# Kernel optimization log

Hardware: AMD Instinct MI355X
Metric: run time of the kernel (lower is better)

The kernel has to match this reference:

```python
import jax, jax.numpy as jnp
import numpy as np

BS, N_STK, N_STK_PNT = 4, 32, 128
N_PNT = N_STK * N_STK_PNT
SP_IN, DN_IN = 128, 128
SP_OUT, DN_OUT = 256, 256
SP_NEAR, DN_NEAR = 2, 10
COOR = 128


def _conv2d(x, w, b, stride=(1, 1), pad='VALID'):
    # x [bs,C,H,W], w [O,I,kh,kw]
    y = jax.lax.conv_general_dilated(x, w, window_strides=stride, padding=pad,
                                     dimension_numbers=('NCHW', 'OIHW', 'NCHW'))
    return y + b[None, :, None, None]


def _fps(xyz, n_sample):
    # farthest point sampling. xyz [bs,n,c] -> [bs,n_sample] int32
    n = xyz.shape[1]

    def one(x):
        def body(i, state):
            idx, dist, far = state
            idx = idx.at[i].set(far)
            d = jnp.sum((x - x[far]) ** 2, axis=-1)
            dist = jnp.minimum(dist, d)
            return idx, dist, jnp.argmax(dist).astype(jnp.int32)

        idx0 = jnp.zeros((n_sample,), jnp.int32)
        dist0 = jnp.full((n,), 1e10, x.dtype)
        idx, _, _ = jax.lax.fori_loop(0, n_sample, body, (idx0, dist0, jnp.int32(0)))
        return idx

    return jax.vmap(one)(xyz)


def _gcn(x, W, b, g, bt, k):
    # DGCNN edge-conv. x [bs,c,n]; W [2c,co]
    xt = jnp.swapaxes(x, 1, 2)                                   # [bs,n,c]
    sq = jnp.sum(xt * xt, axis=-1)                               # [bs,n]
    dist = sq[:, :, None] - 2.0 * jnp.einsum('bnc,bmc->bnm', xt, xt) + sq[:, None, :]
    _, idx = jax.lax.top_k(-dist, k)                             # [bs,n,k]
    nbr = jax.vmap(lambda p, i: p[i])(xt, idx)                   # [bs,n,k,c]
    ctr = jnp.broadcast_to(xt[:, :, None, :], nbr.shape)
    edge = jnp.concatenate([ctr, nbr - ctr], axis=-1)            # [bs,n,k,2c]
    h = jnp.einsum('bnke,eo->bnko', edge, W) + b
    h = jax.nn.relu(g * h + bt)
    return jnp.swapaxes(jnp.max(h, axis=2), 1, 2)                # [bs,co,n]


def setup_inputs() -> dict:
    key = jax.random.key(0)
    ks = jax.random.split(key, 16)
    f32 = jnp.float32
    d = {
        'sparse_fea': jax.random.normal(ks[0], (BS, SP_IN, N_STK), f32),
        'dense_fea': jax.random.normal(ks[1], (BS, DN_IN, N_PNT), f32),
        'stk_coor': jax.random.normal(ks[2], (BS, N_STK, COOR), f32),
        # DenseToSparse: Conv2d(dn_in->dn_in, (1,3)) + BN
        'd2s_w': jax.random.normal(ks[3], (DN_IN, DN_IN, 1, 3), f32) * 0.05,
        'd2s_b': jnp.zeros((DN_IN,), f32),
        'd2s_g': jnp.ones((DN_IN,), f32),
        'd2s_bt': jnp.zeros((DN_IN,), f32),
        # sparse GCN: in = SP_IN + DN_IN, edge feat 2*in
        'sp_W': jax.random.normal(ks[4], (2 * (SP_IN + DN_IN), SP_OUT), f32) * 0.05,
        'sp_b': jnp.zeros((SP_OUT,), f32),
        'sp_g': jnp.ones((SP_OUT,), f32),
        'sp_bt': jnp.zeros((SP_OUT,), f32),
        # dense GCN: in = DN_IN + SP_IN
        'dn_W': jax.random.normal(ks[5], (2 * (DN_IN + SP_IN), DN_OUT), f32) * 0.05,
        'dn_b': jnp.zeros((DN_OUT,), f32),
        'dn_g': jnp.ones((DN_OUT,), f32),
        'dn_bt': jnp.zeros((DN_OUT,), f32),
        # DownSample: Conv2d(dn_out->dn_out, (1,3), stride (1,2), pad (0,1)) + BN
        'ds_w': jax.random.normal(ks[6], (DN_OUT, DN_OUT, 1, 3), f32) * 0.05,
        'ds_b': jnp.zeros((DN_OUT,), f32),
        'ds_g': jnp.ones((DN_OUT,), f32),
        'ds_bt': jnp.zeros((DN_OUT,), f32),
    }
    return d


def reference(sparse_fea, dense_fea, stk_coor,
              d2s_w, d2s_b, d2s_g, d2s_bt,
              sp_W, sp_b, sp_g, sp_bt,
              dn_W, dn_b, dn_g, dn_bt,
              ds_w, ds_b, ds_g, ds_bt):
    bs = sparse_fea.shape[0]
    df = dense_fea.reshape(bs, DN_IN, N_STK, N_STK_PNT)
    # DenseToSparse: conv (1,3) valid + BN(eval) + relu + max over stroke points
    h = _conv2d(df, d2s_w, d2s_b)
    h = jax.nn.relu(d2s_g[None, :, None, None] * h + d2s_bt[None, :, None, None])
    sp_from_dn = jnp.max(h, axis=3)                                    # [bs,dn_in,n_stk]
    union_sparse = jnp.concatenate([sparse_fea, sp_from_dn], axis=1)   # [bs,sp_in+dn_in,n_stk]
    # SparseToDense: broadcast stroke feature onto its points
    dn_from_sp = jnp.broadcast_to(sparse_fea[:, :, :, None], (bs, SP_IN, N_STK, N_STK_PNT))
    union_dense = jnp.concatenate([df, dn_from_sp], axis=1).reshape(bs, DN_IN + SP_IN, N_PNT)
    # GCN (DGCNN edge conv) updates
    sparse_up = _gcn(union_sparse, sp_W, sp_b, sp_g, sp_bt, SP_NEAR)   # [bs,SP_OUT,n_stk]
    dense_up = _gcn(union_dense, dn_W, dn_b, dn_g, dn_bt, DN_NEAR)     # [bs,DN_OUT,n_pnt]
    # DownSample: FPS on stroke coords, gather strokes, strided conv on points
    n_half = N_STK // 2
    fps_idx = _fps(stk_coor, n_half)                                   # [bs,n_half]
    stk_coor_s = jnp.take_along_axis(stk_coor, fps_idx[:, :, None], axis=1)
    sp_s = jnp.take_along_axis(jnp.swapaxes(sparse_up, 1, 2), fps_idx[:, :, None], axis=1)
    sp_s = jnp.swapaxes(sp_s, 1, 2)                                    # [bs,SP_OUT,n_half]
    dn = dense_up.reshape(bs, DN_OUT, N_STK, N_STK_PNT)
    dn = jnp.take_along_axis(dn, fps_idx[:, None, :, None], axis=2)    # [bs,DN_OUT,n_half,n_stk_pnt]
    dn = _conv2d(dn, ds_w, ds_b, stride=(1, 2), pad=[(0, 0), (1, 1)])
    dn = jax.nn.relu(ds_g[None, :, None, None] * dn + ds_bt[None, :, None, None])
    dn = dn.reshape(bs, DN_OUT, n_half * (N_STK_PNT // 2))
    return sp_s, dn, stk_coor_s
```

## Files before the change

### kernel.cpp

```cpp
#include <hip/hip_runtime.h>

#define NPNT 4096
#define NSTK 32

typedef _Float16 half8 __attribute__((ext_vector_type(8)));
typedef float f32x4 __attribute__((ext_vector_type(4)));
typedef unsigned long long u64;

static const size_t OFF_XT   = 0;
static const size_t OFF_P    = 4194304;
static const size_t OFF_Q    = 8388608;
static const size_t OFF_SQD  = 12582912;
static const size_t OFF_SPFD = 12599296;
static const size_t OFF_XS   = 12615680;
static const size_t OFF_PS   = 12648448;
static const size_t OFF_QS   = 12681216;
static const size_t OFF_WSP  = 12746752;
static const size_t OFF_KNN  = 13402112;
static const size_t OFF_IDXS = 13565952;
static const size_t OFF_FPS  = 13566208;
static const size_t OFF_SD   = 13566272;

__device__ __forceinline__ bool lexlt(float d1, int i1, float d2, int i2) {
  return (d1 < d2) || (d1 == d2 && i1 < i2);
}
__device__ __forceinline__ void insert10(float ld[10], int li[10], float d, int i) {
  if (!lexlt(d, i, ld[9], li[9])) return;
  ld[9] = d; li[9] = i;
#pragma unroll
  for (int j = 9; j > 0; j--) {
    if (lexlt(ld[j], li[j], ld[j-1], li[j-1])) {
      float td = ld[j]; ld[j] = ld[j-1]; ld[j-1] = td;
      int ti = li[j]; li[j] = li[j-1]; li[j-1] = ti;
    }
  }
}

__device__ __forceinline__ void insertK(u64 lk[10], u64 k) {
  if (k >= lk[9]) return;
  lk[9] = k;
#pragma unroll
  for (int j = 9; j > 0; j--) {
    u64 a = lk[j-1], b2 = lk[j];
    bool sw = b2 < a;
    lk[j-1] = sw ? b2 : a;
    lk[j]   = sw ? a : b2;
  }
}

#define CASK(a, b) { u64 _x = (a), _y = (b); bool _s = _y < _x; \
  (a) = _s ? _y : _x; (b) = _s ? _x : _y; }

__device__ __forceinline__ void merge10(u64 lk[10], const u64 b[10]) {
  u64 c[10];
#pragma unroll
  for (int i = 0; i < 10; i++) { u64 t = b[9 - i]; u64 a = lk[i]; c[i] = a < t ? a : t; }
  CASK(c[0], c[5]); CASK(c[1], c[6]); CASK(c[2], c[7]); CASK(c[3], c[8]); CASK(c[4], c[9]);
  CASK(c[0], c[1]); CASK(c[1], c[2]); CASK(c[2], c[3]); CASK(c[3], c[4]);
  CASK(c[0], c[1]); CASK(c[1], c[2]); CASK(c[2], c[3]);
  CASK(c[0], c[1]); CASK(c[1], c[2]);
  CASK(c[0], c[1]);
  CASK(c[5], c[6]); CASK(c[6], c[7]); CASK(c[7], c[8]); CASK(c[8], c[9]);
  CASK(c[5], c[6]); CASK(c[6], c[7]); CASK(c[7], c[8]);
  CASK(c[5], c[6]); CASK(c[6], c[7]);
  CASK(c[5], c[6]);
#pragma unroll
  for (int i = 0; i < 10; i++) lk[i] = c[i];
}

__global__ __launch_bounds__(256) void k_split256(const float* __restrict__ df, const float* __restrict__ sf,
    _Float16* __restrict__ XH, _Float16* __restrict__ XL, float* __restrict__ sqd) {
  int b = blockIdx.x, n0 = blockIdx.y * 64;
  int t = threadIdx.x;
  int s0 = n0 >> 7;
  __shared__ float T[128][68];
  __shared__ _Float16 Sh[128], Sl[128];
  {
    int c = t >> 1, nh = (t & 1) * 32;
    const float* src = &df[((size_t)b * 128 + c) * NPNT + n0 + nh];
#pragma unroll
    for (int j = 0; j < 8; j++) *(float4*)&T[c][nh + j * 4] = *(const float4*)&src[j * 4];
  }
  if (t < 128) {
    float x = sf[((size_t)b * 128 + t) * NSTK + s0];
    _Float16 hi = (_Float16)x;
    Sh[t] = hi; Sl[t] = (_Float16)(x - (float)hi);
  }
  __syncthreads();
  {
    int n = t >> 2, cseg = (t & 3) * 32;
    size_t base = ((size_t)b * NPNT + n0 + n) * 256;
    float s = 0.0f;
#pragma unroll
    for (int k = 0; k < 4; k++) {
      half8 hv, lv, shv, slv;
#pragma unroll
      for (int e = 0; e < 8; e++) {
        float x = T[cseg + k * 8 + e][n];
        s = fmaf(x, x, s);
        _Float16 hi = (_Float16)x;
        hv[e] = hi; lv[e] = (_Float16)(x - (float)hi);
        shv[e] = Sh[cseg + k * 8 + e];
        slv[e] = Sl[cseg + k * 8 + e];
      }
      *(half8*)&XH[base + cseg + k * 8] = hv;
      *(half8*)&XL[base + cseg + k * 8] = lv;
      *(half8*)&XH[base + 128 + cseg + k * 8] = shv;
      *(half8*)&XL[base + 128 + cseg + k * 8] = slv;
    }
    s += __shfl_xor(s, 1);
    s += __shfl_xor(s, 2);
    if ((t & 3) == 0) sqd[(size_t)b * NPNT + n0 + n] = s;
  }
}

__global__ __launch_bounds__(256) void k_splitW(const float* __restrict__ W,
    _Float16* __restrict__ WPh, _Float16* __restrict__ WPl,
    _Float16* __restrict__ WQh, _Float16* __restrict__ WQl) {
  int k = blockIdx.x, o = threadIdx.x;
  float w1 = W[(size_t)k * 256 + o];
  float w2 = W[(size_t)(k + 256) * 256 + o];
  float p = w1 - w2;
  _Float16 ph = (_Float16)p;  WPh[(size_t)o * 256 + k] = ph;
  WPl[(size_t)o * 256 + k] = (_Float16)(p - (float)ph);
  _Float16 qh = (_Float16)w2; WQh[(size_t)o * 256 + k] = qh;
  WQl[(size_t)o * 256 + k] = (_Float16)(w2 - (float)qh);
}

__global__ __launch_bounds__(256) void k_d2s(const float* __restrict__ df, const float* __restrict__ w,
    const float* __restrict__ cb, const float* __restrict__ g, const float* __restrict__ bt,
    float* __restrict__ spfd) {
  int b = blockIdx.x, o0 = blockIdx.y * 64, s = blockIdx.z;
  int n0 = s * 128;
  int t = threadIdx.x;
  __shared__ float A[96][64];
  __shared__ float Bs[32][132];
  float acc[4][8];
#pragma unroll
  for (int i = 0; i < 4; i++)
#pragma unroll
    for (int j = 0; j < 8; j++) acc[i][j] = 0.0f;
  int tn = t & 15, to = t >> 4;
  for (int ic = 0; ic < 128; ic += 32) {
    {
      int ol = t >> 2, q = t & 3;
      const float* src = &w[((size_t)(o0 + ol) * 128 + ic) * 3 + q * 24];
#pragma unroll
      for (int r = 0; r < 6; r++) {
        float4 v = *(const float4*)&src[r * 4];
        int e = q * 24 + r * 4;
        A[e+0][ol] = v.x; A[e+1][ol] = v.y; A[e+2][ol] = v.z; A[e+3][ol] = v.w;
      }
    }
    for (int idx = t; idx < 32 * 33; idx += 256) {
      int row = idx / 33, f4 = idx % 33;
      int nb = n0 + f4 * 4;
      const float* srow = &df[((size_t)b * 128 + ic + row) * NPNT];
      float4 v;
      if (nb + 3 < NPNT) v = *(const float4*)&srow[nb];
      else {
        v.x = srow[nb   < NPNT ? nb   : NPNT-1];
        v.y = srow[nb+1 < NPNT ? nb+1 : NPNT-1];
        v.z = srow[nb+2 < NPNT ? nb+2 : NPNT-1];
        v.w = srow[nb+3 < NPNT ? nb+3 : NPNT-1];
      }
      *(float4*)&Bs[row][f4 * 4] = v;
    }
    __syncthreads();
#pragma unroll 2
    for (int ii = 0; ii < 32; ii++) {
      float bv[12];
      *(float4*)&bv[0] = *(const float4*)&Bs[ii][tn * 8];
      *(float4*)&bv[4] = *(const float4*)&Bs[ii][tn * 8 + 4];
      *(float4*)&bv[8] = *(const float4*)&Bs[ii][tn * 8 + 8];
#pragma unroll
      for (int kw = 0; kw < 3; kw++) {
        float4 av = *(const float4*)&A[ii * 3 + kw][to * 4];
#pragma unroll
        for (int j = 0; j < 8; j++) {
          float bvj = bv[kw + j];
          acc[0][j] = fmaf(av.x, bvj, acc[0][j]);
          acc[1][j] = fmaf(av.y, bvj, acc[1][j]);
          acc[2][j] = fmaf(av.z, bvj, acc[2][j]);
          acc[3][j] = fmaf(av.w, bvj, acc[3][j]);
        }
      }
    }
    __syncthreads();
  }
  __shared__ float Dr[64][17];
#pragma unroll
  for (int i = 0; i < 4; i++) {
    int o = o0 + to * 4 + i;
    float gg = g[o], bb = cb[o], bo = bt[o];
    float m = 0.0f;
#pragma unroll
    for (int j = 0; j < 8; j++) {
      int p = tn * 8 + j;
      if (p < 126) {
        float v = fmaf(gg, acc[i][j] + bb, bo);
        v = v > 0.0f ? v : 0.0f;
        m = v > m ? v : m;
      }
    }
    Dr[to * 4 + i][tn] = m;
  }
  __syncthreads();
  if (t < 64) {
    float m = 0.0f;
#pragma unroll
    for (int k = 0; k < 16; k++) m = Dr[t][k] > m ? Dr[t][k] : m;
    spfd[((size_t)b * 128 + o0 + t) * NSTK + s] = m;
  }
}

__global__ __launch_bounds__(128) void k_fps(const float* __restrict__ coor, int* __restrict__ fpsidx,
                                             float* __restrict__ out2) {
  int b = blockIdx.x, t = threadIdx.x;
  __shared__ float X[32][132];
  __shared__ float dist[32];
  __shared__ int far_s;
  __shared__ int sel[16];
  for (int idx = t; idx < 32 * 32; idx += 128) {
    int r = idx >> 5, q = idx & 31;
    *(float4*)&X[r][q * 4] = *(const float4*)&coor[((size_t)b * 32 + r) * 128 + q * 4];
  }
  if (t < 32) dist[t] = 1e10f;
  if (t == 0) far_s = 0;
  __syncthreads();
  for (int it = 0; it < 16; it++) {
    int far = far_s;
    if (t == 0) sel[it] = far;
    if (t < 32) {
      float d = 0.0f;
      for (int c = 0; c < 128; c++) { float dd = X[t][c] - X[far][c]; d = fmaf(dd, dd, d); }
      float dm = dist[t];
      dist[t] = d < dm ? d : dm;
    }
    __syncthreads();
    if (t == 0) {
      float best = -1.0f; int bi = 0;
      for (int m = 0; m < 32; m++) if (dist[m] > best) { best = dist[m]; bi = m; }
      far_s = bi;
    }
    __syncthreads();
  }
  if (t < 16) fpsidx[b * 16 + t] = sel[t];
  __syncthreads();
  for (int idx = t; idx < 16 * 32; idx += 128) {
    int j = idx >> 5, q = idx & 31;
    *(float4*)&out2[((size_t)b * 16 + j) * 128 + q * 4] = *(const float4*)&X[sel[j]][q * 4];
  }
}

__global__ __launch_bounds__(256) void k_sparse_graph(const float* __restrict__ sf, const float* __restrict__ spfd,
    float* __restrict__ xs, int* __restrict__ idxs, float* __restrict__ SD) {
  int b = blockIdx.x, t = threadIdx.x;
  __shared__ float X[32][260];
  __shared__ float sq[32];
  __shared__ float D[32][33];
  for (int idx = t; idx < 32 * 256; idx += 256) {
    int n = idx >> 8, c = idx & 255;
    float v = (c < 128) ? sf[((size_t)b * 128 + c) * NSTK + n]
                        : spfd[((size_t)b * 128 + (c - 128)) * NSTK + n];
    X[n][c] = v;
  }
  __syncthreads();
  for (int idx = t; idx < 32 * 64; idx += 256) {
    int n = idx >> 6, q = idx & 63;
    *(float4*)&xs[((size_t)b * 32 + n) * 256 + q * 4] = *(const float4*)&X[n][q * 4];
  }
#pragma unroll
  for (int rep = 0; rep < 4; rep++) {
    int p = t + rep * 256;
    int s = p >> 5, u = p & 31;
    float acc = 0.0f;
    for (int c = 0; c < 128; c++) {
      float d = X[s][c] - X[u][c];
      acc = fmaf(d, d, acc);
    }
    SD[(size_t)b * 1024 + p] = acc;
  }
  if (t < 32) {
    float s = 0.0f;
    for (int c = 0; c < 256; c++) s = fmaf(X[t][c], X[t][c], s);
    sq[t] = s;
  }
  __syncthreads();
  {
    int n = t >> 3;
    for (int mg = 0; mg < 4; mg++) {
      int m = (t & 7) + mg * 8;
      float dot = 0.0f;
      for (int c = 0; c < 256; c++) dot = fmaf(X[n][c], X[m][c], dot);
      D[n][m] = (sq[n] - 2.0f * dot) + sq[m];
    }
  }
  __syncthreads();
  if (t < 32) {
    float d0 = 1e30f, d1 = 1e30f; int i0 = 0, i1 = 0;
    for (int m = 0; m < 32; m++) {
      float d = D[t][m];
      if (d < d0) { d1 = d0; i1 = i0; d0 = d; i0 = m; }
      else if (d < d1) { d1 = d; i1 = m; }
    }
    idxs[(b * 32 + t) * 2 + 0] = i0;
    idxs[(b * 32 + t) * 2 + 1] = i1;
  }
}

__global__ __launch_bounds__(256) void k_sparse_pq(const float* __restrict__ xs, const float* __restrict__ W,
    float* __restrict__ Ps, float* __restrict__ Qs) {
  int b = blockIdx.x >> 5, n = blockIdx.x & 31;
  int o = threadIdx.x;
  const float* xr = &xs[((size_t)b * 32 + n) * 256];
  float accP = 0.0f, accQ = 0.0f;
  for (int c = 0; c < 256; c++) {
    float xc = xr[c];
    float w1 = W[(size_t)c * 256 + o];
    float w2 = W[(size_t)(c + 256) * 256 + o];
    accP = fmaf(xc, w1 - w2, accP);
    accQ = fmaf(xc, w2, accQ);
  }
  Ps[((size_t)b * 32 + n) * 256 + o] = accP;
  Qs[((size_t)b * 32 + n) * 256 + o] = accQ;
}

__global__ __launch_bounds__(256) void k_sparse_cg(const float* __restrict__ Ps, const float* __restrict__ Qs,
    const int* __restrict__ idxs, const int* __restrict__ fps,
    const float* __restrict__ g, const float* __restrict__ cb, const float* __restrict__ bt,
    float* __restrict__ out0) {
  int b = blockIdx.x, j = blockIdx.y, o = threadIdx.x;
  int n = fps[b * 16 + j];
  int i0 = idxs[(b * 32 + n) * 2 + 0], i1 = idxs[(b * 32 + n) * 2 + 1];
  float p = Ps[((size_t)b * 32 + n) * 256 + o];
  float q0 = Qs[((size_t)b * 32 + i0) * 256 + o];
  float q1 = Qs[((size_t)b * 32 + i1) * 256 + o];
  float gg = g[o], bb = cb[o], bo = bt[o];
  float h0 = fmaf(gg, p + q0 + bb, bo); h0 = h0 > 0.0f ? h0 : 0.0f;
  float h1 = fmaf(gg, p + q1 + bb, bo); h1 = h1 > 0.0f ? h1 : 0.0f;
  out0[((size_t)b * 256 + o) * 16 + j] = h0 > h1 ? h0 : h1;
}

#define STAGE(ch2_, p_) { \
  int srow = t >> 2, scol = (t & 3) * 16; \
  size_t gp = (bofs + (size_t)(m0 + (ch2_) * 64 + srow)) * 256 + (p_) * 64 + scol; \
  float4 gh0 = *(const float4*)&XH[gp]; float4 gh1 = *(const float4*)&XH[gp + 8]; \
  float4 gl0 = *(const float4*)&XL[gp]; float4 gl1 = *(const float4*)&XL[gp + 8]; \
  int lo = srow * 72 + scol; \
  *(float4*)&BshH[lo] = gh0; *(float4*)&BshH[lo + 8] = gh1; \
  *(float4*)&BshL[lo] = gl0; *(float4*)&BshL[lo + 8] = gl1; }

#define DWU(wv_, r_, c_) DwU[(((wv_) * 16 + (r_)) * 68) + (c_)]

__global__ __launch_bounds__(256, 4) void k_knn_mfma(const _Float16* __restrict__ XH,
    const _Float16* __restrict__ XL, const float* __restrict__ sqd, const float* __restrict__ SD,
    const int* __restrict__ fps, u64* __restrict__ pk) {
  const int h = blockIdx.x, rb = blockIdx.y, b = blockIdx.z;
  const int t = threadIdx.x;
  const int w = t >> 6, L = t & 63;
  const int c15 = L & 15, q = L >> 4;
  const int jst = rb >> 1;
  const int ph = (rb & 1) * 64;
  const int s_stk = fps[b * 16 + jst];
  const int nsrc = s_stk * 128 + ph + w * 16;
  const int rc0 = rb * 64 + w * 16;
  const size_t bofs = (size_t)b * NPNT;

  __shared__ __align__(16) char SMEM[18432];
  _Float16* const BshH = (_Float16*)SMEM;
  _Float16* const BshL = (_Float16*)(SMEM + 64 * 72 * 2);
  unsigned* const DwU = (unsigned*)SMEM;

  half8 ah[4], al[4];
  {
    const _Float16* ap  = XH + (bofs + nsrc + c15) * 256 + q * 8;
    const _Float16* apl = XL + (bofs + nsrc + c15) * 256 + q * 8;
#pragma unroll
    for (int ch = 0; ch < 4; ch++) {
      ah[ch] = *(const half8*)(ap + ch * 32);
      al[ch] = *(const half8*)(apl + ch * 32);
    }
  }
  float snr[4];
#pragma unroll
  for (int r = 0; r < 4; r++) snr[r] = sqd[bofs + nsrc + q * 4 + r];

  u64 lk[10];
#pragma unroll
  for (int j = 0; j < 10; j++) lk[j] = ~0ull;

  const bool own_here = ((s_stk >> 1) == h);
  const int r_sel = L >> 2, sl = L & 3;
  const int u0 = own_here ? s_stk : (h * 2);
  const int u1 = own_here ? (s_stk ^ 1) : (h * 2 + 1);

#pragma unroll 1
  for (int it = 0; it < 2; it++) {
    const int u = (it == 0) ? u0 : u1;
    const int m0 = u * 128;
    const float SDv = SD[((size_t)b * 32 + s_stk) * 32 + u];

#pragma unroll 1
    for (int ch2 = 0; ch2 < 2; ch2++) {
      float smv[4];
#pragma unroll
      for (int cg = 0; cg < 4; cg++) smv[cg] = sqd[bofs + m0 + ch2 * 64 + cg * 16 + c15];

      f32x4 zz = {0.0f, 0.0f, 0.0f, 0.0f};
      f32x4 acc[4];
#pragma unroll
      for (int cg = 0; cg < 4; cg++) acc[cg] = zz;

      __syncthreads();
      STAGE(ch2, 0);
      __syncthreads();
#pragma unroll
      for (int chl = 0; chl < 2; chl++) {
#pragma unroll
        for (int cg = 0; cg < 4; cg++) {
          int lo = (cg * 16 + c15) * 72 + chl * 32 + q * 8;
          half8 bh = *(const half8*)&BshH[lo];
          half8 bl = *(const half8*)&BshL[lo];
          acc[cg] = __builtin_amdgcn_mfma_f32_16x16x32_f16(ah[chl], bh, acc[cg], 0, 0, 0);
          acc[cg] = __builtin_amdgcn_mfma_f32_16x16x32_f16(ah[chl], bl, acc[cg], 0, 0, 0);
          acc[cg] = __builtin_amdgcn_mfma_f32_16x16x32_f16(al[chl], bh, acc[cg], 0, 0, 0);
        }
      }
      __syncthreads();
      STAGE(ch2, 1);
      __syncthreads();
#pragma unroll
      for (int chl = 0; chl < 2; chl++) {
#pragma unroll
        for (int cg = 0; cg < 4; cg++) {
          int lo = (cg * 16 + c15) * 72 + chl * 32 + q * 8;
          half8 bh = *(const half8*)&BshH[lo];
          half8 bl = *(const half8*)&BshL[lo];
          acc[cg] = __builtin_amdgcn_mfma_f32_16x16x32_f16(ah[2 + chl], bh, acc[cg], 0, 0, 0);
          acc[cg] = __builtin_amdgcn_mfma_f32_16x16x32_f16(ah[2 + chl], bl, acc[cg], 0, 0, 0);
          acc[cg] = __builtin_amdgcn_mfma_f32_16x16x32_f16(al[2 + chl], bh, acc[cg], 0, 0, 0);
        }
      }
      __syncthreads();

#pragma unroll
      for (int cg = 0; cg < 4; cg++) {
        float basec = SDv + smv[cg];
#pragma unroll
        for (int r = 0; r < 4; r++) {
          float d = fmaf(-2.0f, acc[cg][r], snr[r] + basec);
          unsigned uu = __float_as_uint(d);
          unsigned kk = uu ^ ((unsigned)((int)uu >> 31) | 0x80000000u);
          DWU(w, q * 4 + r, cg * 16 + c15) = kk;
        }
      }
#pragma unroll
      for (int jj = 0; jj < 4; jj++) {
        uint4 kv = *(const uint4*)&DWU(w, r_sel, jj * 16 + sl * 4);
        int ib = m0 + ch2 * 64 + jj * 16 + sl * 4;
        insertK(lk, ((u64)kv.x << 32) | (unsigned)(ib + 0));
        insertK(lk, ((u64)kv.y << 32) | (unsigned)(ib + 1));
        insertK(lk, ((u64)kv.z << 32) | (unsigned)(ib + 2));
        insertK(lk, ((u64)kv.w << 32) | (unsigned)(ib + 3));
      }
    }
  }

#pragma unroll
  for (int m = 1; m <= 2; m <<= 1) {
    u64 o[10];
#pragma unroll
    for (int j = 0; j < 10; j++) o[j] = __shfl_xor(lk[j], m);
    merge10(lk, o);
  }
  if (sl == 0) {
    size_t row = (size_t)b * 2048 + rc0 + r_sel;
    u64* dst = &pk[(row * 16 + h) * 10];
#pragma unroll
    for (int j = 0; j < 10; j++) dst[j] = lk[j];
  }
}

__global__ __launch_bounds__(256) void k_knn_merge(const u64* __restrict__ pk,
                                                   int* __restrict__ knnc) {
  size_t row = blockIdx.x * 256 + threadIdx.x;
  const u64* src = &pk[row * 160];
  u64 lk[10];
#pragma unroll
  for (int j = 0; j < 10; j++) lk[j] = src[j];
#pragma unroll
  for (int l = 1; l < 16; l++) {
    u64 bv[10];
#pragma unroll
    for (int j = 0; j < 10; j++) bv[j] = src[l * 10 + j];
    merge10(lk, bv);
  }
#pragma unroll
  for (int j = 0; j < 10; j++) knnc[row * 10 + j] = (int)(unsigned)(lk[j] & 0xffffffffull);
}

__global__ __launch_bounds__(256, 2) void k_pq_mfma(const _Float16* __restrict__ XH, const _Float16* __restrict__ XL,
    const _Float16* __restrict__ WPh, const _Float16* __restrict__ WPl,
    const _Float16* __restrict__ WQh, const _Float16* __restrict__ WQl,
    const int* __restrict__ fps, const float* __restrict__ g, const float* __restrict__ cb,
    const float* __restrict__ bt, float* __restrict__ Pc, float* __restrict__ Qp) {
  const int b = blockIdx.z;
  const int t = threadIdx.x, w = t >> 6, L = t & 63;
  const int c15 = L & 15, q = L >> 4;
  const int ow = blockIdx.y * 128 + (w >> 1) * 64;
  const size_t bofs = (size_t)b * NPNT;
  f32x4 zz = {0.0f, 0.0f, 0.0f, 0.0f};

  {
    const int nw = blockIdx.x * 32 + (w & 1) * 16;
    f32x4 accQ[4];
#pragma unroll
    for (int cg = 0; cg < 4; cg++) accQ[cg] = zz;
    const _Float16* ap  = XH + (bofs + nw + c15) * 256 + q * 8;
    const _Float16* apl = XL + (bofs + nw + c15) * 256 + q * 8;
#pragma unroll
    for (int ch = 0; ch < 8; ch++) {
      half8 a_h = *(const half8*)(ap + ch * 32);
      half8 a_l = *(const half8*)(apl + ch * 32);
#pragma unroll
      for (int cg = 0; cg < 4; cg++) {
        size_t wb = (size_t)(ow + cg * 16 + c15) * 256 + ch * 32 + q * 8;
        half8 bqh = *(const half8*)(WQh + wb);
        half8 bql = *(const half8*)(WQl + wb);
        accQ[cg] = __builtin_amdgcn_mfma_f32_16x16x32_f16(a_h, bqh, accQ[cg], 0, 0, 0);
        accQ[cg] = __builtin_amdgcn_mfma_f32_16x16x32_f16(a_h, bql, accQ[cg], 0, 0, 0);
        accQ[cg] = __builtin_amdgcn_mfma_f32_16x16x32_f16(a_l, bqh, accQ[cg], 0, 0, 0);
      }
    }
#pragma unroll
    for (int cg = 0; cg < 4; cg++) {
      int o = ow + cg * 16 + c15;
      float gg = g[o];
#pragma unroll
      for (int r = 0; r < 4; r++) {
        Qp[(bofs + nw + q * 4 + r) * 256 + o] = gg * accQ[cg][r];
      }
    }
  }

  if (blockIdx.x < 64) {
    const int m0 = blockIdx.x * 32 + (w & 1) * 16;
    const int jst = m0 >> 7;
    const int pbase = m0 & 127;
    const int nsrc = fps[b * 16 + jst] * 128 + pbase;
    f32x4 accP[4];
#pragma unroll
    for (int cg = 0; cg < 4; cg++) accP[cg] = zz;
    const _Float16* ap  = XH + (bofs + nsrc + c15) * 256 + q * 8;
    const _Float16* apl = XL + (bofs + nsrc + c15) * 256 + q * 8;
#pragma unroll
    for (int ch = 0; ch < 8; ch++) {
      half8 a_h = *(const half8*)(ap + ch * 32);
      half8 a_l = *(const half8*)(apl + ch * 32);
#pragma unroll
      for (int cg = 0; cg < 4; cg++) {
        size_t wb = (size_t)(ow + cg * 16 + c15) * 256 + ch * 32 + q * 8;
        half8 bph = *(const half8*)(WPh + wb);
        half8 bpl = *(const half8*)(WPl + wb);
        accP[cg] = __builtin_amdgcn_mfma_f32_16x16x32_f16(a_h, bph, accP[cg], 0, 0, 0);
        accP[cg] = __builtin_amdgcn_mfma_f32_16x16x32_f16(a_h, bpl, accP[cg], 0, 0, 0);
        accP[cg] = __builtin_amdgcn_mfma_f32_16x16x32_f16(a_l, bph, accP[cg], 0, 0, 0);
      }
    }
#pragma unroll
    for (int cg = 0; cg < 4; cg++) {
      int o = ow + cg * 16 + c15;
      float gg = g[o], bb = cb[o], bo = bt[o];
#pragma unroll
      for (int r = 0; r < 4; r++) {
        Pc[(((size_t)b * 16 + jst) * 128 + pbase + q * 4 + r) * 256 + o] =
            fmaf(gg, accP[cg][r] + bb, bo);
      }
    }
  }
}

__global__ __launch_bounds__(256) void k_build_E(const float* __restrict__ Pc, const float* __restrict__ Qp,
    const int* __restrict__ knnc, float* __restrict__ E) {
  int pp = blockIdx.x, j = blockIdx.y, b = blockIdx.z;
  int t = threadIdx.x;
  float v[3];
#pragma unroll
  for (int dp = 0; dp < 3; dp++) {
    int p = 2 * pp - 1 + dp;
    float val = 0.0f;
    if (p >= 0 && p < 128) {
      size_t m = ((size_t)b * 16 + j) * 128 + p;
      float pv = Pc[m * 256 + t];
      const int* id = &knnc[m * 10];
      float mx = 0.0f;
#pragma unroll
      for (int k = 0; k < 10; k++) {
        float qv = Qp[((size_t)b * NPNT + id[k]) * 256 + t];
        float h = pv + qv;
        mx = h > mx ? h : mx;
      }
      val = mx;
    }
    v[dp] = val;
  }
  size_t base = ((size_t)(b * 16 + j) * 64 + pp) * 768;
  E[base + 3 * t + 0] = v[0];
  E[base + 3 * t + 1] = v[1];
  E[base + 3 * t + 2] = v[2];
}

__global__ __launch_bounds__(256) void k_ds_gemm(const float* __restrict__ Wd, const float* __restrict__ E,
    const float* __restrict__ cb, const float* __restrict__ g, const float* __restrict__ bt,
    float* __restrict__ out1) {
  int j0 = blockIdx.x * 64, o0 = blockIdx.y * 64, b = blockIdx.z;
  int t = threadIdx.x;
  __shared__ float A[32][68];
  __shared__ float Bs[32][68];
  float acc[4][4];
#pragma unroll
  for (int i = 0; i < 4; i++)
#pragma unroll
    for (int j = 0; j < 4; j++) acc[i][j] = 0.0f;
  int tj = t & 15, to = t >> 4;
  for (int kc = 0; kc < 768; kc += 32) {
    {
      int ol = t >> 2, q = t & 3;
      const float* src = &Wd[(size_t)(o0 + ol) * 768 + kc + q * 8];
      float4 v0 = *(const float4*)src, v1 = *(const float4*)(src + 4);
      int cc = q * 8;
      A[cc+0][ol] = v0.x; A[cc+1][ol] = v0.y; A[cc+2][ol] = v0.z; A[cc+3][ol] = v0.w;
      A[cc+4][ol] = v1.x; A[cc+5][ol] = v1.y; A[cc+6][ol] = v1.z; A[cc+7][ol] = v1.w;
    }
    {
      int jl = t >> 2, q = t & 3;
      const float* src = &E[((size_t)b * 1024 + j0 + jl) * 768 + kc + q * 8];
      float4 v0 = *(const float4*)src, v1 = *(const float4*)(src + 4);
      int cc = q * 8;
      Bs[cc+0][jl] = v0.x; Bs[cc+1][jl] = v0.y; Bs[cc+2][jl] = v0.z; Bs[cc+3][jl] = v0.w;
      Bs[cc+4][jl] = v1.x; Bs[cc+5][jl] = v1.y; Bs[cc+6][jl] = v1.z; Bs[cc+7][jl] = v1.w;
    }
    __syncthreads();
#pragma unroll 4
    for (int k = 0; k < 32; k++) {
      float4 a = *(const float4*)&A[k][to * 4];
      float4 bv = *(const float4*)&Bs[k][tj * 4];
      float av[4] = {a.x, a.y, a.z, a.w};
      float bb[4] = {bv.x, bv.y, bv.z, bv.w};
#pragma unroll
      for (int i = 0; i < 4; i++)
#pragma unroll
        for (int j = 0; j < 4; j++)
          acc[i][j] = fmaf(av[i], bb[j], acc[i][j]);
    }
    __syncthreads();
  }
#pragma unroll
  for (int i = 0; i < 4; i++) {
    int o = o0 + to * 4 + i;
    float gg = g[o], bb = cb[o], bo = bt[o];
    float4 v;
    float x0 = fmaf(gg, acc[i][0] + bb, bo); v.x = x0 > 0.0f ? x0 : 0.0f;
    float x1 = fmaf(gg, acc[i][1] + bb, bo); v.y = x1 > 0.0f ? x1 : 0.0f;
    float x2 = fmaf(gg, acc[i][2] + bb, bo); v.z = x2 > 0.0f ? x2 : 0.0f;
    float x3 = fmaf(gg, acc[i][3] + bb, bo); v.w = x3 > 0.0f ? x3 : 0.0f;
    *(float4*)&out1[((size_t)b * 256 + o) * 1024 + j0 + tj * 4] = v;
  }
}

extern "C" void kernel_launch(void* const* d_in, const int* in_sizes, int n_in,
                              void* d_out, int out_size, void* d_ws, size_t ws_size,
                              hipStream_t stream) {
  (void)in_sizes; (void)n_in; (void)out_size; (void)ws_size;
  const float* sf    = (const float*)d_in[0];
  const float* df    = (const float*)d_in[1];
  const float* coor  = (const float*)d_in[2];
  const float* d2sw  = (const float*)d_in[3];
  const float* d2sb  = (const float*)d_in[4];
  const float* d2sg  = (const float*)d_in[5];
  const float* d2sbt = (const float*)d_in[6];
  const float* spW   = (const float*)d_in[7];
  const float* spb   = (const float*)d_in[8];
  const float* spg   = (const float*)d_in[9];
  const float* spbt  = (const float*)d_in[10];
  const float* dnW   = (const float*)d_in[11];
  const float* dnb   = (const float*)d_in[12];
  const float* dng   = (const float*)d_in[13];
  const float* dnbt  = (const float*)d_in[14];
  const float* dsw   = (const float*)d_in[15];
  const float* dsb   = (const float*)d_in[16];
  const float* dsg   = (const float*)d_in[17];
  const float* dsbt  = (const float*)d_in[18];

  float* ws   = (float*)d_ws;
  float* Pc   = ws + OFF_P;
  float* Qp   = ws + OFF_Q;
  float* SQD  = ws + OFF_SQD;
  float* SPFD = ws + OFF_SPFD;
  float* XS   = ws + OFF_XS;
  float* PS   = ws + OFF_PS;
  float* QS   = ws + OFF_QS;
  int*   KNNC = (int*)(ws + OFF_KNN);
  int*   IDXS = (int*)(ws + OFF_IDXS);
  int*   FPS  = (int*)(ws + OFF_FPS);
  float* SD   = ws + OFF_SD;
  _Float16* XT2H = (_Float16*)(ws + OFF_XT);
  _Float16* XT2L = XT2H + (size_t)4 * NPNT * 256;
  float* E = ws + OFF_XT;
  _Float16* WPh = (_Float16*)(ws + OFF_WSP);
  _Float16* WPl = WPh + 65536;
  _Float16* WQh = WPh + 131072;
  _Float16* WQl = WPh + 196608;
  u64* PK = (u64*)(ws + OFF_Q);

  float* out0 = (float*)d_out;
  float* out1 = out0 + 16384;
  float* out2 = out1 + 1048576;

  k_split256<<<dim3(4, 64), 256, 0, stream>>>(df, sf, XT2H, XT2L, SQD);
  k_splitW<<<dim3(256), 256, 0, stream>>>(dnW, WPh, WPl, WQh, WQl);
  k_d2s<<<dim3(4, 2, 32), 256, 0, stream>>>(df, d2sw, d2sb, d2sg, d2sbt, SPFD);
  k_fps<<<dim3(4), 128, 0, stream>>>(coor, FPS, out2);
  k_sparse_graph<<<dim3(4), 256, 0, stream>>>(sf, SPFD, XS, IDXS, SD);
  k_sparse_pq<<<dim3(128), 256, 0, stream>>>(XS, spW, PS, QS);
  k_sparse_cg<<<dim3(4, 16), 256, 0, stream>>>(PS, QS, IDXS, FPS, spg, spb, spbt, out0);
  k_knn_mfma<<<dim3(16, 32, 4), 256, 0, stream>>>(XT2H, XT2L, SQD, SD, FPS, PK);
  k_knn_merge<<<dim3(32), 256, 0, stream>>>(PK, KNNC);
  k_pq_mfma<<<dim3(128, 2, 4), 256, 0, stream>>>(XT2H, XT2L, WPh, WPl, WQh, WQl,
                                                 FPS, dng, dnb, dnbt, Pc, Qp);
  k_build_E<<<dim3(64, 16, 4), 256, 0, stream>>>(Pc, Qp, KNNC, E);
  k_ds_gemm<<<dim3(16, 4, 4), 256, 0, stream>>>(dsw, E, dsb, dsg, dsbt, out1);
}
```

Measured before the change: 455.7 us.

## Fuse four preprocessing kernels into one launch and parallelize kNN merge across lanes

Merges the split, weight-split, dense-to-sparse conv and FPS kernels into a single k_pre kernel that dispatches on block index, so the four independent jobs share one launch and run concurrently. It also spreads the 16-way partial top-10 merge in k_knn_merge over four lanes per row with shuffle-based merges, giving 4x more threads. The fused kernel's shared memory is sized for the largest branch, which may reduce occupancy for the lighter branches, and the serial FPS blocks now sit in the same grid as the others.

```diff
diff --git a/kernel.cpp b/kernel.cpp
--- a/kernel.cpp
+++ b/kernel.cpp
@@ -21,21 +21,6 @@
 static const size_t OFF_FPS  = 13566208;
 static const size_t OFF_SD   = 13566272;
 
-__device__ __forceinline__ bool lexlt(float d1, int i1, float d2, int i2) {
-  return (d1 < d2) || (d1 == d2 && i1 < i2);
-}
-__device__ __forceinline__ void insert10(float ld[10], int li[10], float d, int i) {
-  if (!lexlt(d, i, ld[9], li[9])) return;
-  ld[9] = d; li[9] = i;
-#pragma unroll
-  for (int j = 9; j > 0; j--) {
-    if (lexlt(ld[j], li[j], ld[j-1], li[j-1])) {
-      float td = ld[j]; ld[j] = ld[j-1]; ld[j-1] = td;
-      int ti = li[j]; li[j] = li[j-1]; li[j-1] = ti;
-    }
-  }
-}
-
 __device__ __forceinline__ void insertK(u64 lk[10], u64 k) {
   if (k >= lk[9]) return;
   lk[9] = k;
@@ -68,188 +53,191 @@
   for (int i = 0; i < 10; i++) lk[i] = c[i];
 }
 
-__global__ __launch_bounds__(256) void k_split256(const float* __restrict__ df, const float* __restrict__ sf,
-    _Float16* __restrict__ XH, _Float16* __restrict__ XL, float* __restrict__ sqd) {
-  int b = blockIdx.x, n0 = blockIdx.y * 64;
-  int t = threadIdx.x;
-  int s0 = n0 >> 7;
-  __shared__ float T[128][68];
-  __shared__ _Float16 Sh[128], Sl[128];
-  {
-    int c = t >> 1, nh = (t & 1) * 32;
-    const float* src = &df[((size_t)b * 128 + c) * NPNT + n0 + nh];
-#pragma unroll
-    for (int j = 0; j < 8; j++) *(float4*)&T[c][nh + j * 4] = *(const float4*)&src[j * 4];
-  }
-  if (t < 128) {
-    float x = sf[((size_t)b * 128 + t) * NSTK + s0];
-    _Float16 hi = (_Float16)x;
-    Sh[t] = hi; Sl[t] = (_Float16)(x - (float)hi);
-  }
-  __syncthreads();
-  {
-    int n = t >> 2, cseg = (t & 3) * 32;
-    size_t base = ((size_t)b * NPNT + n0 + n) * 256;
-    float s = 0.0f;
-#pragma unroll
-    for (int k = 0; k < 4; k++) {
-      half8 hv, lv, shv, slv;
-#pragma unroll
-      for (int e = 0; e < 8; e++) {
-        float x = T[cseg + k * 8 + e][n];
-        s = fmaf(x, x, s);
-        _Float16 hi = (_Float16)x;
-        hv[e] = hi; lv[e] = (_Float16)(x - (float)hi);
-        shv[e] = Sh[cseg + k * 8 + e];
-        slv[e] = Sl[cseg + k * 8 + e];
-      }
-      *(half8*)&XH[base + cseg + k * 8] = hv;
-      *(half8*)&XL[base + cseg + k * 8] = lv;
-      *(half8*)&XH[base + 128 + cseg + k * 8] = shv;
-      *(half8*)&XL[base + 128 + cseg + k * 8] = slv;
-    }
-    s += __shfl_xor(s, 1);
-    s += __shfl_xor(s, 2);
-    if ((t & 3) == 0) sqd[(size_t)b * NPNT + n0 + n] = s;
-  }
-}
-
-__global__ __launch_bounds__(256) void k_splitW(const float* __restrict__ W,
+__global__ __launch_bounds__(256) void k_pre(
+    const float* __restrict__ df, const float* __restrict__ sf,
+    const float* __restrict__ coor, const float* __restrict__ dnW,
+    const float* __restrict__ d2sw, const float* __restrict__ d2scb,
+    const float* __restrict__ d2sg, const float* __restrict__ d2sbt,
+    _Float16* __restrict__ XH, _Float16* __restrict__ XL, float* __restrict__ sqd,
     _Float16* __restrict__ WPh, _Float16* __restrict__ WPl,
-    _Float16* __restrict__ WQh, _Float16* __restrict__ WQl) {
-  int k = blockIdx.x, o = threadIdx.x;
-  float w1 = W[(size_t)k * 256 + o];
-  float w2 = W[(size_t)(k + 256) * 256 + o];
-  float p = w1 - w2;
-  _Float16 ph = (_Float16)p;  WPh[(size_t)o * 256 + k] = ph;
-  WPl[(size_t)o * 256 + k] = (_Float16)(p - (float)ph);
-  _Float16 qh = (_Float16)w2; WQh[(size_t)o * 256 + k] = qh;
-  WQl[(size_t)o * 256 + k] = (_Float16)(w2 - (float)qh);
-}
-
-__global__ __launch_bounds__(256) void k_d2s(const float* __restrict__ df, const float* __restrict__ w,
-    const float* __restrict__ cb, const float* __restrict__ g, const float* __restrict__ bt,
-    float* __restrict__ spfd) {
-  int b = blockIdx.x, o0 = blockIdx.y * 64, s = blockIdx.z;
-  int n0 = s * 128;
-  int t = threadIdx.x;
-  __shared__ float A[96][64];
-  __shared__ float Bs[32][132];
-  float acc[4][8];
-#pragma unroll
-  for (int i = 0; i < 4; i++)
-#pragma unroll
-    for (int j = 0; j < 8; j++) acc[i][j] = 0.0f;
-  int tn = t & 15, to = t >> 4;
-  for (int ic = 0; ic < 128; ic += 32) {
+    _Float16* __restrict__ WQh, _Float16* __restrict__ WQl,
+    float* __restrict__ spfd, int* __restrict__ fpsidx, float* __restrict__ out2) {
+  __shared__ __align__(16) char SMEM[46080];
+  const int bid = blockIdx.x;
+  const int t = threadIdx.x;
+
+  if (bid < 4) {
+    int b = bid;
+    float (*X)[132] = (float (*)[132])SMEM;
+    float* dist = (float*)(SMEM + 16896);
+    int* far_s  = (int*)(SMEM + 17024);
+    int* sel    = (int*)(SMEM + 17028);
+    for (int idx = t; idx < 32 * 32; idx += 256) {
+      int r = idx >> 5, q = idx & 31;
+      *(float4*)&X[r][q * 4] = *(const float4*)&coor[((size_t)b * 32 + r) * 128 + q * 4];
+    }
+    if (t < 32) dist[t] = 1e10f;
+    if (t == 0) *far_s = 0;
+    __syncthreads();
+    for (int it = 0; it < 16; it++) {
+      int far = *far_s;
+      if (t == 0) sel[it] = far;
+      if (t < 32) {
+        float d = 0.0f;
+        for (int c = 0; c < 128; c++) { float dd = X[t][c] - X[far][c]; d = fmaf(dd, dd, d); }
+        float dm = dist[t];
+        dist[t] = d < dm ? d : dm;
+      }
+      __syncthreads();
+      if (t == 0) {
+        float best = -1.0f; int bi = 0;
+        for (int m = 0; m < 32; m++) if (dist[m] > best) { best = dist[m]; bi = m; }
+        *far_s = bi;
+      }
+      __syncthreads();
+    }
+    if (t < 16) fpsidx[b * 16 + t] = sel[t];
+    __syncthreads();
+    for (int idx = t; idx < 16 * 32; idx += 256) {
+      int j = idx >> 5, q = idx & 31;
+      *(float4*)&out2[((size_t)b * 16 + j) * 128 + q * 4] = *(const float4*)&X[sel[j]][q * 4];
+    }
+  } else if (bid < 260) {
+    int idx0 = bid - 4;
+    int b = idx0 & 3, n0 = (idx0 >> 2) * 64;
+    int s0 = n0 >> 7;
+    float (*T)[68] = (float (*)[68])SMEM;
+    _Float16* Sh = (_Float16*)(SMEM + 34816);
+    _Float16* Sl = (_Float16*)(SMEM + 35072);
     {
-      int ol = t >> 2, q = t & 3;
-      const float* src = &w[((size_t)(o0 + ol) * 128 + ic) * 3 + q * 24];
-#pragma unroll
-      for (int r = 0; r < 6; r++) {
-        float4 v = *(const float4*)&src[r * 4];
-        int e = q * 24 + r * 4;
-        A[e+0][ol] = v.x; A[e+1][ol] = v.y; A[e+2][ol] = v.z; A[e+3][ol] = v.w;
-      }
-    }
-    for (int idx = t; idx < 32 * 33; idx += 256) {
-      int row = idx / 33, f4 = idx % 33;
-      int nb = n0 + f4 * 4;
-      const float* srow = &df[((size_t)b * 128 + ic + row) * NPNT];
-      float4 v;
-      if (nb + 3 < NPNT) v = *(const float4*)&srow[nb];
-      else {
-        v.x = srow[nb   < NPNT ? nb   : NPNT-1];
-        v.y = srow[nb+1 < NPNT ? nb+1 : NPNT-1];
-        v.z = srow[nb+2 < NPNT ? nb+2 : NPNT-1];
-        v.w = srow[nb+3 < NPNT ? nb+3 : NPNT-1];
-      }
-      *(float4*)&Bs[row][f4 * 4] = v;
+      int c = t >> 1, nh = (t & 1) * 32;
+      const float* src = &df[((size_t)b * 128 + c) * NPNT + n0 + nh];
+#pragma unroll
+      for (int j = 0; j < 8; j++) *(float4*)&T[c][nh + j * 4] = *(const float4*)&src[j * 4];
+    }
+    if (t < 128) {
+      float x = sf[((size_t)b * 128 + t) * NSTK + s0];
+      _Float16 hi = (_Float16)x;
+      Sh[t] = hi; Sl[t] = (_Float16)(x - (float)hi);
     }
     __syncthreads();
+    {
+      int n = t >> 2, cseg = (t & 3) * 32;
+      size_t base = ((size_t)b * NPNT + n0 + n) * 256;
+      float s = 0.0f;
+#pragma unroll
+      for (int k = 0; k < 4; k++) {
+        half8 hv, lv, shv, slv;
+#pragma unroll
+        for (int e = 0; e < 8; e++) {
+          float x = T[cseg + k * 8 + e][n];
+          s = fmaf(x, x, s);
+          _Float16 hi = (_Float16)x;
+          hv[e] = hi; lv[e] = (_Float16)(x - (float)hi);
+          shv[e] = Sh[cseg + k * 8 + e];
+          slv[e] = Sl[cseg + k * 8 + e];
+        }
+        *(half8*)&XH[base + cseg + k * 8] = hv;
+        *(half8*)&XL[base + cseg + k * 8] = lv;
+        *(half8*)&XH[base + 128 + cseg + k * 8] = shv;
+        *(half8*)&XL[base + 128 + cseg + k * 8] = slv;
+      }
+      s += __shfl_xor(s, 1);
+      s += __shfl_xor(s, 2);
+      if ((t & 3) == 0) sqd[(size_t)b * NPNT + n0 + n] = s;
+    }
+  } else if (bid < 516) {
+    int idx0 = bid - 260;
+    int b = idx0 & 3, o0 = ((idx0 >> 2) & 1) * 64, s = idx0 >> 3;
+    int n0 = s * 128;
+    float (*A)[64]   = (float (*)[64])SMEM;
+    float (*Bs)[132] = (float (*)[132])(SMEM + 24576);
+    float (*Dr)[17]  = (float (*)[17])(SMEM + 41472);
+    float acc[4][8];
+#pragma unroll
+    for (int i = 0; i < 4; i++)
+#pragma unroll
+      for (int j = 0; j < 8; j++) acc[i][j] = 0.0f;
+    int tn = t & 15, to = t >> 4;
+    for (int ic = 0; ic < 128; ic += 32) {
+      {
+        int ol = t >> 2, q = t & 3;
+        const float* src = &d2sw[((size_t)(o0 + ol) * 128 + ic) * 3 + q * 24];
+#pragma unroll
+        for (int r = 0; r < 6; r++) {
+          float4 v = *(const float4*)&src[r * 4];
+          int e = q * 24 + r * 4;
+          A[e+0][ol] = v.x; A[e+1][ol] = v.y; A[e+2][ol] = v.z; A[e+3][ol] = v.w;
+        }
+      }
+      for (int idx = t; idx < 32 * 33; idx += 256) {
+        int row = idx / 33, f4 = idx % 33;
+        int nb = n0 + f4 * 4;
+        const float* srow = &df[((size_t)b * 128 + ic + row) * NPNT];
+        float4 v;
+        if (nb + 3 < NPNT) v = *(const float4*)&srow[nb];
+        else {
+          v.x = srow[nb   < NPNT ? nb   : NPNT-1];
+          v.y = srow[nb+1 < NPNT ? nb+1 : NPNT-1];
+          v.z = srow[nb+2 < NPNT ? nb+2 : NPNT-1];
+          v.w = srow[nb+3 < NPNT ? nb+3 : NPNT-1];
+        }
+        *(float4*)&Bs[row][f4 * 4] = v;
+      }
+      __syncthreads();
 #pragma unroll 2
-    for (int ii = 0; ii < 32; ii++) {
-      float bv[12];
-      *(float4*)&bv[0] = *(const float4*)&Bs[ii][tn * 8];
-      *(float4*)&bv[4] = *(const float4*)&Bs[ii][tn * 8 + 4];
-      *(float4*)&bv[8] = *(const float4*)&Bs[ii][tn * 8 + 8];
-#pragma unroll
-      for (int kw = 0; kw < 3; kw++) {
-        float4 av = *(const float4*)&A[ii * 3 + kw][to * 4];
-#pragma unroll
-        for (int j = 0; j < 8; j++) {
-          float bvj = bv[kw + j];
-          acc[0][j] = fmaf(av.x, bvj, acc[0][j]);
-          acc[1][j] = fmaf(av.y, bvj, acc[1][j]);
-          acc[2][j] = fmaf(av.z, bvj, acc[2][j]);
-          acc[3][j] = fmaf(av.w, bvj, acc[3][j]);
+      for (int ii = 0; ii < 32; ii++) {
+        float bv[12];
+        *(float4*)&bv[0] = *(const float4*)&Bs[ii][tn * 8];
+        *(float4*)&bv[4] = *(const float4*)&Bs[ii][tn * 8 + 4];
+        *(float4*)&bv[8] = *(const float4*)&Bs[ii][tn * 8 + 8];
+#pragma unroll
+        for (int kw = 0; kw < 3; kw++) {
+          float4 av = *(const float4*)&A[ii * 3 + kw][to * 4];
+#pragma unroll
+          for (int j = 0; j < 8; j++) {
+            float bvj = bv[kw + j];
+            acc[0][j] = fmaf(av.x, bvj, acc[0][j]);
+            acc[1][j] = fmaf(av.y, bvj, acc[1][j]);
+            acc[2][j] = fmaf(av.z, bvj, acc[2][j]);
+            acc[3][j] = fmaf(av.w, bvj, acc[3][j]);
+          }
         }
       }
+      __syncthreads();
+    }
+#pragma unroll
+    for (int i = 0; i < 4; i++) {
+      int o = o0 + to * 4 + i;
+      float gg = d2sg[o], bb = d2scb[o], bo = d2sbt[o];
+      float m = 0.0f;
+#pragma unroll
+      for (int j = 0; j < 8; j++) {
+        int p = tn * 8 + j;
+        if (p < 126) {
+          float v = fmaf(gg, acc[i][j] + bb, bo);
+          v = v > 0.0f ? v : 0.0f;
+          m = v > m ? v : m;
+        }
+      }
+      Dr[to * 4 + i][tn] = m;
     }
     __syncthreads();
-  }
-  __shared__ float Dr[64][17];
-#pragma unroll
-  for (int i = 0; i < 4; i++) {
-    int o = o0 + to * 4 + i;
-    float gg = g[o], bb = cb[o], bo = bt[o];
-    float m = 0.0f;
-#pragma unroll
-    for (int j = 0; j < 8; j++) {
-      int p = tn * 8 + j;
-      if (p < 126) {
-        float v = fmaf(gg, acc[i][j] + bb, bo);
-        v = v > 0.0f ? v : 0.0f;
-        m = v > m ? v : m;
-      }
-    }
-    Dr[to * 4 + i][tn] = m;
-  }
-  __syncthreads();
-  if (t < 64) {
-    float m = 0.0f;
-#pragma unroll
-    for (int k = 0; k < 16; k++) m = Dr[t][k] > m ? Dr[t][k] : m;
-    spfd[((size_t)b * 128 + o0 + t) * NSTK + s] = m;
-  }
-}
-
-__global__ __launch_bounds__(128) void k_fps(const float* __restrict__ coor, int* __restrict__ fpsidx,
-                                             float* __restrict__ out2) {
-  int b = blockIdx.x, t = threadIdx.x;
-  __shared__ float X[32][132];
-  __shared__ float dist[32];
-  __shared__ int far_s;
-  __shared__ int sel[16];
-  for (int idx = t; idx < 32 * 32; idx += 128) {
-    int r = idx >> 5, q = idx & 31;
-    *(float4*)&X[r][q * 4] = *(const float4*)&coor[((size_t)b * 32 + r) * 128 + q * 4];
-  }
-  if (t < 32) dist[t] = 1e10f;
-  if (t == 0) far_s = 0;
-  __syncthreads();
-  for (int it = 0; it < 16; it++) {
-    int far = far_s;
-    if (t == 0) sel[it] = far;
-    if (t < 32) {
-      float d = 0.0f;
-      for (int c = 0; c < 128; c++) { float dd = X[t][c] - X[far][c]; d = fmaf(dd, dd, d); }
-      float dm = dist[t];
-      dist[t] = d < dm ? d : dm;
-    }
-    __syncthreads();
-    if (t == 0) {
-      float best = -1.0f; int bi = 0;
-      for (int m = 0; m < 32; m++) if (dist[m] > best) { best = dist[m]; bi = m; }
-      far_s = bi;
-    }
-    __syncthreads();
-  }
-  if (t < 16) fpsidx[b * 16 + t] = sel[t];
-  __syncthreads();
-  for (int idx = t; idx < 16 * 32; idx += 128) {
-    int j = idx >> 5, q = idx & 31;
-    *(float4*)&out2[((size_t)b * 16 + j) * 128 + q * 4] = *(const float4*)&X[sel[j]][q * 4];
+    if (t < 64) {
+      float m = 0.0f;
+#pragma unroll
+      for (int k = 0; k < 16; k++) m = Dr[t][k] > m ? Dr[t][k] : m;
+      spfd[((size_t)b * 128 + o0 + t) * NSTK + s] = m;
+    }
+  } else {
+    int k = bid - 516, o = t;
+    float w1 = dnW[(size_t)k * 256 + o];
+    float w2 = dnW[(size_t)(k + 256) * 256 + o];
+    float p = w1 - w2;
+    _Float16 ph = (_Float16)p;  WPh[(size_t)o * 256 + k] = ph;
+    WPl[(size_t)o * 256 + k] = (_Float16)(p - (float)ph);
+    _Float16 qh = (_Float16)w2; WQh[(size_t)o * 256 + k] = qh;
+    WQl[(size_t)o * 256 + k] = (_Float16)(w2 - (float)qh);
   }
 }
 
@@ -484,20 +472,31 @@
 
 __global__ __launch_bounds__(256) void k_knn_merge(const u64* __restrict__ pk,
                                                    int* __restrict__ knnc) {
-  size_t row = blockIdx.x * 256 + threadIdx.x;
-  const u64* src = &pk[row * 160];
+  int gid = blockIdx.x * 256 + threadIdx.x;
+  size_t row = (size_t)(gid >> 2);
+  int sl = gid & 3;
+  const u64* src = &pk[row * 160 + (size_t)sl * 40];
   u64 lk[10];
 #pragma unroll
   for (int j = 0; j < 10; j++) lk[j] = src[j];
 #pragma unroll
-  for (int l = 1; l < 16; l++) {
+  for (int l = 1; l < 4; l++) {
     u64 bv[10];
 #pragma unroll
     for (int j = 0; j < 10; j++) bv[j] = src[l * 10 + j];
     merge10(lk, bv);
   }
 #pragma unroll
-  for (int j = 0; j < 10; j++) knnc[row * 10 + j] = (int)(unsigned)(lk[j] & 0xffffffffull);
+  for (int m = 1; m <= 2; m <<= 1) {
+    u64 o[10];
+#pragma unroll
+    for (int j = 0; j < 10; j++) o[j] = __shfl_xor(lk[j], m);
+    merge10(lk, o);
+  }
+  if (sl == 0) {
+#pragma unroll
+    for (int j = 0; j < 10; j++) knnc[row * 10 + j] = (int)(unsigned)(lk[j] & 0xffffffffull);
+  }
 }
 
 __global__ __launch_bounds__(256, 2) void k_pq_mfma(const _Float16* __restrict__ XH, const _Float16* __restrict__ XL,
@@ -718,15 +717,14 @@
   float* out1 = out0 + 16384;
   float* out2 = out1 + 1048576;
 
-  k_split256<<<dim3(4, 64), 256, 0, stream>>>(df, sf, XT2H, XT2L, SQD);
-  k_splitW<<<dim3(256), 256, 0, stream>>>(dnW, WPh, WPl, WQh, WQl);
-  k_d2s<<<dim3(4, 2, 32), 256, 0, stream>>>(df, d2sw, d2sb, d2sg, d2sbt, SPFD);
-  k_fps<<<dim3(4), 128, 0, stream>>>(coor, FPS, out2);
+  k_pre<<<dim3(772), 256, 0, stream>>>(df, sf, coor, dnW, d2sw, d2sb, d2sg, d2sbt,
+                                       XT2H, XT2L, SQD, WPh, WPl, WQh, WQl,
+                                       SPFD, FPS, out2);
   k_sparse_graph<<<dim3(4), 256, 0, stream>>>(sf, SPFD, XS, IDXS, SD);
   k_sparse_pq<<<dim3(128), 256, 0, stream>>>(XS, spW, PS, QS);
   k_sparse_cg<<<dim3(4, 16), 256, 0, stream>>>(PS, QS, IDXS, FPS, spg, spb, spbt, out0);
   k_knn_mfma<<<dim3(16, 32, 4), 256, 0, stream>>>(XT2H, XT2L, SQD, SD, FPS, PK);
-  k_knn_merge<<<dim3(32), 256, 0, stream>>>(PK, KNNC);
+  k_knn_merge<<<dim3(128), 256, 0, stream>>>(PK, KNNC);
   k_pq_mfma<<<dim3(128, 2, 4), 256, 0, stream>>>(XT2H, XT2L, WPh, WPl, WQh, WQl,
                                                  FPS, dng, dnb, dnbt, Pc, Qp);
   k_build_E<<<dim3(64, 16, 4), 256, 0, stream>>>(Pc, Qp, KNNC, E);
```

After: 411.9 us. 1.11x faster.
